# Kernel optimization log

Hardware: AMD Instinct MI355X
Metric: run time of the kernel (lower is better)

The kernel has to match this reference:

```python
import jax, jax.numpy as jnp
import numpy as np

B, TC, TP = 2, 1024, 512
NVC, NVP = 8, 4
D, K, H, DFF, L, HOR, NQ = 128, 3, 8, 512, 2, 96, 3
DK = D // H
MASK_VAL = -1e4  # finite stand-in for -inf; entmax15 support never reaches entries this far below the row max


def entmax15(z):
    # Exact 1.5-entmax over the last axis (Peters & Martins sort-based algorithm).
    z = z / 2.0
    z = z - jnp.max(z, axis=-1, keepdims=True)
    zs = jnp.flip(jnp.sort(z, axis=-1), axis=-1)  # descending
    kk = jnp.arange(1, z.shape[-1] + 1, dtype=z.dtype)
    mean = jnp.cumsum(zs, axis=-1) / kk
    meansq = jnp.cumsum(zs * zs, axis=-1) / kk
    ss = kk * (meansq - mean * mean)
    delta = (1.0 - ss) / kk
    pos = delta > 0
    sqrt_d = jnp.where(pos, jnp.sqrt(jnp.where(pos, delta, 1.0)), 0.0)  # grad-safe sqrt
    tau = mean - sqrt_d
    support = jnp.sum((tau <= zs).astype(jnp.int32), axis=-1, keepdims=True)
    tau_star = jnp.take_along_axis(tau, support - 1, axis=-1)
    return jnp.square(jnp.clip(z - tau_star, 0.0, None))


def layer_norm(x, g, b, eps=1e-5):
    m = jnp.mean(x, axis=-1, keepdims=True)
    v = jnp.mean(jnp.square(x - m), axis=-1, keepdims=True)
    return (x - m) * jax.lax.rsqrt(v + eps) * g + b


def selector(x, conv_w, conv_b, sel_w, sel_b, key):
    # x: [B, T, nv]; causal depthwise-grouped conv -> per-var local states [B, T, nv, D]
    Bs, T, nv = x.shape
    xc = jnp.transpose(x, (0, 2, 1))  # [B, nv, T]
    out = jax.lax.conv_general_dilated(
        xc, conv_w, window_strides=(1,), padding=[(K - 1, 0)],
        dimension_numbers=('NCH', 'OIH', 'NCH'), feature_group_count=nv)
    ls = out.reshape(Bs, nv, D, T) + conv_b[None, :, :, None]
    ls = jnp.transpose(ls, (0, 3, 1, 2))  # [B, T, nv, D]
    scores = ls @ sel_w + sel_b  # [B, T, nv]
    scores = jnp.clip(scores, -10.0, 10.0)
    scores = scores + 1e-4 * jax.random.normal(key, scores.shape, scores.dtype)
    w = entmax15(scores)  # [B, T, nv]
    weighted = jnp.sum(ls * w[..., None], axis=2)  # [B, T, D]
    return weighted, w


def attn_block(x, Wq, bq, Wk, bk, Wv, bv, Wo, bo):
    Bs, T, _ = x.shape
    q = (x @ Wq + bq).reshape(Bs, T, H, DK)
    k = (x @ Wk + bk).reshape(Bs, T, H, DK)
    v = (x @ Wv + bv).reshape(Bs, T, H, DK)
    scores = jnp.einsum('bthd,bshd->bhts', q, k) / jnp.sqrt(jnp.float32(DK))
    mask = jnp.triu(jnp.ones((T, T), bool), 1)
    scores = jnp.where(mask[None, None], MASK_VAL, scores)
    w = entmax15(scores)            # [B, H, T, T]
    w_avg = jnp.mean(w, axis=1)     # [B, T, T]
    v_comb = jnp.mean(v, axis=2)    # [B, T, DK]
    out = jnp.einsum('bts,bsd->btd', w_avg, v_comb)
    return out @ Wo + bo, w_avg


def forward(x_cond, x_pred, cw_c, cb_c, sw_c, sb_c, cw_p, cb_p, sw_p, sb_p,
            Wq, bq, Wk, bk, Wv, bv, Wo, bo, ln1_g, ln1_b,
            fw1, fb1, fw2, fb2, ln2_g, ln2_b, proj_w, proj_b):
    nk = jax.random.key(42)
    xc, v_cond = selector(x_cond, cw_c, cb_c, sw_c, sb_c, jax.random.fold_in(nk, 0))
    xp, v_pred = selector(x_pred, cw_p, cb_p, sw_p, sb_p, jax.random.fold_in(nk, 1))
    x = jnp.concatenate([xc, xp], axis=1)  # [B, TC+TP, D]
    logs = []
    for l in range(L):
        a, w = attn_block(x, Wq[l], bq[l], Wk[l], bk[l], Wv[l], bv[l], Wo[l], bo[l])
        x = layer_norm(x + a, ln1_g[l], ln1_b[l])
        h = jax.nn.relu(x @ fw1[l] + fb1[l])
        x = layer_norm(h @ fw2[l] + fb2[l] + x, ln2_g[l], ln2_b[l])
        logs.append(w)
    seq_last = x[:, -1, :]
    out = jnp.einsum('bd,qdh->bqh', seq_last, proj_w) + proj_b  # [B, NQ, HOR]
    return out, v_cond, v_pred, jnp.stack(logs)


def setup_inputs():
    key = jax.random.key(0)
    ks = jax.random.split(key, 16)
    def w(i, shp):
        return (0.02 * jax.random.normal(ks[i], shp)).astype(jnp.float32)
    z = lambda shp: jnp.zeros(shp, jnp.float32)
    o = lambda shp: jnp.ones(shp, jnp.float32)
    return {
        'x_cond': jax.random.normal(ks[0], (B, TC, NVC), jnp.float32),
        'x_pred': jax.random.normal(ks[1], (B, TP, NVP), jnp.float32),
        'cw_c': w(2, (NVC * D, 1, K)), 'cb_c': z((NVC, D)),
        'sw_c': w(3, (D,)), 'sb_c': z((1,)),
        'cw_p': w(4, (NVP * D, 1, K)), 'cb_p': z((NVP, D)),
        'sw_p': w(5, (D,)), 'sb_p': z((1,)),
        'Wq': w(6, (L, D, D)), 'bq': z((L, D)),
        'Wk': w(7, (L, D, D)), 'bk': z((L, D)),
        'Wv': w(8, (L, D, D)), 'bv': z((L, D)),
        'Wo': w(9, (L, DK, D)), 'bo': z((L, D)),
        'ln1_g': o((L, D)), 'ln1_b': z((L, D)),
        'fw1': w(10, (L, D, DFF)), 'fb1': z((L, DFF)),
        'fw2': w(11, (L, DFF, D)), 'fb2': z((L, D)),
        'ln2_g': o((L, D)), 'ln2_b': z((L, D)),
        'proj_w': w(12, (NQ, D, HOR)), 'proj_b': z((NQ, HOR)),
    }


def reference(x_cond, x_pred, cw_c, cb_c, sw_c, sb_c, cw_p, cb_p, sw_p, sb_p,
              Wq, bq, Wk, bk, Wv, bv, Wo, bo, ln1_g, ln1_b,
              fw1, fb1, fw2, fb2, ln2_g, ln2_b, proj_w, proj_b):
    return forward(x_cond, x_pred, cw_c, cb_c, sw_c, sb_c, cw_p, cb_p, sw_p, sb_p,
                   Wq, bq, Wk, bk, Wv, bv, Wo, bo, ln1_g, ln1_b,
                   fw1, fb1, fw2, fb2, ln2_g, ln2_b, proj_w, proj_b)
```

## Files before the change

kernel.cpp:

```cpp
#include <hip/hip_runtime.h>

namespace {

constexpr int NB_  = 2;
constexpr int TC_  = 1024;
constexpr int TP_  = 512;
constexpr int TT_  = 1536;
constexpr int D_   = 128;
constexpr int H_   = 8;
constexpr int DK_  = 16;
constexpr int DFF_ = 512;
constexpr int L_   = 2;
constexpr int HOR_ = 96;
constexpr int NQ_  = 3;

constexpr int SCP_ = TT_ + 8;

typedef _Float16 h2 __attribute__((ext_vector_type(2)));

constexpr int OFF_OUT  = 0;
constexpr int OFF_VC   = NB_ * NQ_ * HOR_;
constexpr int OFF_VP   = OFF_VC + NB_ * TC_ * 8;
constexpr int OFF_LOGS = OFF_VP + NB_ * TP_ * 4;

constexpr int WS_XA  = 0;
constexpr int WS_XB  = WS_XA  + NB_ * TT_ * D_;
constexpr int WS_Q16 = WS_XB  + NB_ * TT_ * D_;
constexpr int WS_K16 = WS_Q16 + NB_ * TT_ * D_ / 2;
constexpr int WS_VC  = WS_K16 + NB_ * TT_ * D_ / 2;
constexpr int WS_WVC = WS_VC  + NB_ * TT_ * DK_;
constexpr int WS_BVC = WS_WVC + L_ * D_ * DK_;

__device__ inline float dot2f(h2 a, h2 b, float c) {
#if __has_builtin(__builtin_amdgcn_fdot2)
    return __builtin_amdgcn_fdot2(a, b, c, false);
#else
    return c + (float)a[0] * (float)b[0] + (float)a[1] * (float)b[1];
#endif
}

__device__ inline unsigned pack2h(float a, float b) {
#if __has_builtin(__builtin_amdgcn_cvt_pkrtz)
    return __builtin_bit_cast(unsigned, __builtin_amdgcn_cvt_pkrtz(a, b));
#else
    h2 p; p[0] = (_Float16)a; p[1] = (_Float16)b;
    return __builtin_bit_cast(unsigned, p);
#endif
}

__device__ inline float fast_rcp(float x) {
#if __has_builtin(__builtin_amdgcn_rcpf)
    return __builtin_amdgcn_rcpf(x);
#else
    return 1.0f / x;
#endif
}

template <int CTRL>
__device__ inline float dpp_add(float x) {
    const int y = __builtin_amdgcn_update_dpp(
        0, __builtin_bit_cast(int, x), CTRL, 0xF, 0xF, true);
    return x + __builtin_bit_cast(float, y);
}
template <int CTRL>
__device__ inline float dpp_maxf(float x) {
    const int y = __builtin_amdgcn_update_dpp(
        __builtin_bit_cast(int, x), __builtin_bit_cast(int, x),
        CTRL, 0xF, 0xF, false);
    return fmaxf(x, __builtin_bit_cast(float, y));
}
__device__ inline float bcast63(float x) {
    return __builtin_bit_cast(float,
        __builtin_amdgcn_readlane(__builtin_bit_cast(int, x), 63));
}
__device__ inline float wave_sum_l63(float x) {
    x = dpp_add<0x111>(x); x = dpp_add<0x112>(x); x = dpp_add<0x114>(x);
    x = dpp_add<0x118>(x); x = dpp_add<0x142>(x); x = dpp_add<0x143>(x);
    return x;
}
__device__ inline float wave_sum(float x) { return bcast63(wave_sum_l63(x)); }
__device__ inline float wave_max(float x) {
    x = dpp_maxf<0x111>(x); x = dpp_maxf<0x112>(x); x = dpp_maxf<0x114>(x);
    x = dpp_maxf<0x118>(x); x = dpp_maxf<0x142>(x); x = dpp_maxf<0x143>(x);
    return bcast63(x);
}

__global__ __launch_bounds__(128) void prep_wvc_kernel(
    const float* __restrict__ Wv, const float* __restrict__ bv,
    float* __restrict__ wvc, float* __restrict__ bvc)
{
    const int l = blockIdx.x;
    const float* W  = Wv + (long)l * D_ * D_;
    const float* bb = bv + l * D_;
    float* wv = wvc + l * D_ * DK_;
    float* bo = bvc + l * DK_;
    const int tid = threadIdx.x;
    for (int idx = tid; idx < D_ * DK_; idx += 128) {
        const int i = idx >> 4, dk = idx & 15;
        float s = 0.f;
        #pragma unroll
        for (int hh = 0; hh < H_; ++hh) s += W[i * D_ + hh * DK_ + dk];
        wv[idx] = s * 0.125f;
    }
    if (tid < DK_) {
        float s = 0.f;
        #pragma unroll
        for (int hh = 0; hh < H_; ++hh) s += bb[hh * DK_ + tid];
        bo[tid] = s * 0.125f;
    }
}

template <int NV>
__device__ inline void selector_qkv_body(
    const float* __restrict__ x, const float* __restrict__ cw,
    const float* __restrict__ cb, const float* __restrict__ sw,
    const float* __restrict__ sb, float* __restrict__ vout,
    float* __restrict__ xout, int Tsel, int row_off, int blk,
    const float* __restrict__ Wq, const float* __restrict__ bq,
    const float* __restrict__ Wk, const float* __restrict__ bk,
    const float* __restrict__ wvc, const float* __restrict__ bvc,
    _Float16* __restrict__ q16, _Float16* __restrict__ k16,
    float* __restrict__ vc)
{
    const int tpb = Tsel / 4;
    const int b   = blk / tpb;
    const int t0  = (blk - b * tpb) * 4;
    const int tid = threadIdx.x;
    const int lane = tid & 63, wave = tid >> 6;
    const int t = t0 + wave;

    __shared__ float xrT[D_][4];

    const int d0 = lane, d1 = lane + 64;
    float xw[3 * NV];
    #pragma unroll
    for (int kk = 0; kk < 3; ++kk) {
        const int ts = t + kk - 2;
        #pragma unroll
        for (int v = 0; v < NV; ++v)
            xw[kk * NV + v] = (ts >= 0) ? x[((long)b * Tsel + ts) * NV + v] : 0.0f;
    }
    float ls0[NV], ls1[NV];
    #pragma unroll
    for (int v = 0; v < NV; ++v) {
        const float* c0 = cw + ((long)(v * D_ + d0)) * 3;
        const float* c1 = cw + ((long)(v * D_ + d1)) * 3;
        float a0 = cb[v * D_ + d0], a1 = cb[v * D_ + d1];
        a0 = fmaf(xw[0*NV+v], c0[0], a0); a1 = fmaf(xw[0*NV+v], c1[0], a1);
        a0 = fmaf(xw[1*NV+v], c0[1], a0); a1 = fmaf(xw[1*NV+v], c1[1], a1);
        a0 = fmaf(xw[2*NV+v], c0[2], a0); a1 = fmaf(xw[2*NV+v], c1[2], a1);
        ls0[v] = a0; ls1[v] = a1;
    }
    float u[NV];
    {
        const float s0 = sw[d0], s1 = sw[d1];
        #pragma unroll
        for (int v = 0; v < NV; ++v)
            u[v] = wave_sum(fmaf(ls1[v], s1, ls0[v] * s0));
    }
    float wls[NV];
    {
        float m = -1e30f;
        #pragma unroll
        for (int v = 0; v < NV; ++v) {
            float s = u[v] + sb[0];
            s = fminf(fmaxf(s, -10.0f), 10.0f);
            u[v] = 0.5f * s;
            m = fmaxf(m, u[v]);
        }
        float tau = m - 1.0f;
        for (int it = 0; it < 12; ++it) {
            float S1 = 0.f, S2 = 0.f;
            #pragma unroll
            for (int v = 0; v < NV; ++v) {
                float dd = fmaxf(u[v] - tau, 0.f);
                S1 += dd; S2 = fmaf(dd, dd, S2);
            }
            tau += (S2 - 1.0f) * 0.5f * fast_rcp(S1);
        }
        float S1 = 0.f, S2 = 0.f, K = 0.f;
        #pragma unroll
        for (int v = 0; v < NV; ++v) {
            if (u[v] > tau) { S1 += u[v]; S2 = fmaf(u[v], u[v], S2); K += 1.f; }
        }
        const float mean = S1 / K;
        const float arg  = fmaxf(fmaf(mean, mean, -(S2 - 1.0f) / K), 0.f);
        tau = mean - sqrtf(arg);
        #pragma unroll
        for (int v = 0; v < NV; ++v) {
            const float dd = fmaxf(u[v] - tau, 0.f);
            wls[v] = dd * dd;
        }
    }
    float acc0 = 0.f, acc1 = 0.f;
    #pragma unroll
    for (int v = 0; v < NV; ++v) {
        acc0 = fmaf(ls0[v], wls[v], acc0);
        acc1 = fmaf(ls1[v], wls[v], acc1);
    }
    const long rowb = (long)b * TT_ + row_off + t0;
    const long row  = rowb + wave;
    xout[row * D_ + d0] = acc0;
    xout[row * D_ + d1] = acc1;
    xrT[d0][wave] = acc0;
    xrT[d1][wave] = acc1;
    if (lane == 0) {
        #pragma unroll
        for (int v = 0; v < NV; ++v)
            vout[((long)b * Tsel + t) * NV + v] = wls[v];
    }
    __syncthreads();

    {
        const int c = tid & 127;
        const int which = tid >> 7;
        const float* __restrict__ W = which ? Wk : Wq;
        const float bb = which ? bk[c] : bq[c];
        float a0 = bb, a1 = bb, a2 = bb, a3 = bb;
        for (int i = 0; i < D_; ++i) {
            const float wv = W[i * D_ + c];
            const float4 xv = *(const float4*)&xrT[i][0];
            a0 = fmaf(xv.x, wv, a0);
            a1 = fmaf(xv.y, wv, a1);
            a2 = fmaf(xv.z, wv, a2);
            a3 = fmaf(xv.w, wv, a3);
        }
        _Float16* __restrict__ dst = which ? k16 : q16;
        dst[(rowb + 0) * D_ + c] = (_Float16)a0;
        dst[(rowb + 1) * D_ + c] = (_Float16)a1;
        dst[(rowb + 2) * D_ + c] = (_Float16)a2;
        dst[(rowb + 3) * D_ + c] = (_Float16)a3;
    }
    if (tid < 64) {
        const int r = tid >> 4, c16 = tid & 15;
        float av = bvc[c16];
        for (int i = 0; i < D_; ++i)
            av = fmaf(xrT[i][r], wvc[i * DK_ + c16], av);
        vc[(rowb + r) * DK_ + c16] = av;
    }
}

__global__ __launch_bounds__(256) void pre_kernel(
    const float* __restrict__ x_cond, const float* __restrict__ cw_c,
    const float* __restrict__ cb_c, const float* __restrict__ sw_c,
    const float* __restrict__ sb_c,
    const float* __restrict__ x_pred, const float* __restrict__ cw_p,
    const float* __restrict__ cb_p, const float* __restrict__ sw_p,
    const float* __restrict__ sb_p,
    float* __restrict__ vc_out, float* __restrict__ vp_out,
    float* __restrict__ xout,
    const float* __restrict__ Wq, const float* __restrict__ bq,
    const float* __restrict__ Wk, const float* __restrict__ bk,
    const float* __restrict__ wvc, const float* __restrict__ bvc,
    _Float16* __restrict__ q16, _Float16* __restrict__ k16,
    float* __restrict__ vc)
{
    const int blk = blockIdx.x;
    if (blk < NB_ * TC_ / 4) {
        selector_qkv_body<8>(x_cond, cw_c, cb_c, sw_c, sb_c, vc_out, xout,
                             TC_, 0, blk, Wq, bq, Wk, bk, wvc, bvc,
                             q16, k16, vc);
    } else {
        selector_qkv_body<4>(x_pred, cw_p, cb_p, sw_p, sb_p, vp_out, xout,
                             TP_, TC_, blk - NB_ * TC_ / 4,
                             Wq, bq, Wk, bk, wvc, bvc, q16, k16, vc);
    }
}

template <int NJ>
__device__ inline void entmax_head2(unsigned short* __restrict__ sa,
                                    unsigned short* __restrict__ sb,
                                    int lane, int t)
{
    const unsigned* __restrict__ rpa = (const unsigned*)sa;
    const unsigned* __restrict__ rpb = (const unsigned*)sb;
    float va[2 * NJ], vb[2 * NJ];
    #pragma unroll
    for (int j = 0; j < NJ; ++j) {
        const unsigned dwa = rpa[64 * j + lane];
        const unsigned dwb = rpb[64 * j + lane];
        const h2 ha = __builtin_bit_cast(h2, dwa);
        const h2 hb = __builtin_bit_cast(h2, dwb);
        const int s0 = 128 * j + 2 * lane;
        const bool in0 = (s0 <= t), in1 = (s0 + 1 <= t);
        va[2*j]   = in0 ? (float)ha[0] : -1e30f;
        va[2*j+1] = in1 ? (float)ha[1] : -1e30f;
        vb[2*j]   = in0 ? (float)hb[0] : -1e30f;
        vb[2*j+1] = in1 ? (float)hb[1] : -1e30f;
    }

    float ma0 = va[0], ma1 = va[1], mb0 = vb[0], mb1 = vb[1];
    #pragma unroll
    for (int j = 2; j < 2 * NJ; j += 2) {
        ma0 = fmaxf(ma0, va[j]); ma1 = fmaxf(ma1, va[j+1]);
        mb0 = fmaxf(mb0, vb[j]); mb1 = fmaxf(mb1, vb[j+1]);
    }
    const float ma = wave_max(fmaxf(ma0, ma1));
    const float mb = wave_max(fmaxf(mb0, mb1));

    float ta = ma - 1.0f, tb = mb - 1.0f;
    #pragma unroll
    for (int it = 0; it < 7; ++it) {
        float a10 = 0.f, a11 = 0.f, a20 = 0.f, a21 = 0.f;
        float b10 = 0.f, b11 = 0.f, b20 = 0.f, b21 = 0.f;
        #pragma unroll
        for (int j = 0; j < 2 * NJ; j += 2) {
            const float da0 = fmaxf(va[j]   - ta, 0.f);
            const float da1 = fmaxf(va[j+1] - ta, 0.f);
            const float db0 = fmaxf(vb[j]   - tb, 0.f);
            const float db1 = fmaxf(vb[j+1] - tb, 0.f);
            a10 += da0; a11 += da1;
            a20 = fmaf(da0, da0, a20); a21 = fmaf(da1, da1, a21);
            b10 += db0; b11 += db1;
            b20 = fmaf(db0, db0, b20); b21 = fmaf(db1, db1, b21);
        }
        const float S1a = wave_sum(a10 + a11);
        const float S2a = wave_sum(a20 + a21);
        const float S1b = wave_sum(b10 + b11);
        const float S2b = wave_sum(b20 + b21);
        ta += (S2a - 1.0f) * 0.5f * fast_rcp(S1a);
        tb += (S2b - 1.0f) * 0.5f * fast_rcp(S1b);
    }
    {
        float a1 = 0.f, a2 = 0.f, ka = 0.f;
        float b1 = 0.f, b2 = 0.f, kb = 0.f;
        #pragma unroll
        for (int j = 0; j < 2 * NJ; ++j) {
            if (va[j] > ta) { a1 += va[j]; a2 = fmaf(va[j], va[j], a2); ka += 1.f; }
            if (vb[j] > tb) { b1 += vb[j]; b2 = fmaf(vb[j], vb[j], b2); kb += 1.f; }
        }
        a1 = wave_sum(a1); a2 = wave_sum(a2); ka = wave_sum(ka);
        b1 = wave_sum(b1); b2 = wave_sum(b2); kb = wave_sum(kb);
        const float meana = a1 / ka;
        const float arga  = fmaxf(fmaf(meana, meana, -(a2 - 1.0f) / ka), 0.f);
        ta = meana - sqrtf(arga);
        const float meanb = b1 / kb;
        const float argb  = fmaxf(fmaf(meanb, meanb, -(b2 - 1.0f) / kb), 0.f);
        tb = meanb - sqrtf(argb);
    }
    unsigned* __restrict__ wpa = (unsigned*)sa;
    unsigned* __restrict__ wpb = (unsigned*)sb;
    #pragma unroll
    for (int j = 0; j < NJ; ++j) {
        const float da0 = fmaxf(va[2*j]   - ta, 0.f);
        const float da1 = fmaxf(va[2*j+1] - ta, 0.f);
        const float db0 = fmaxf(vb[2*j]   - tb, 0.f);
        const float db1 = fmaxf(vb[2*j+1] - tb, 0.f);
        wpa[64 * j + lane] = pack2h(da0 * da0, da1 * da1);
        wpb[64 * j + lane] = pack2h(db0 * db0, db1 * db1);
    }
}

template <int NJ>
__device__ inline void entmax_pair(unsigned short* __restrict__ scb,
                                   int wave, int lane, int t)
{
    entmax_head2<NJ>(scb + (wave * 2 + 0) * SCP_,
                     scb + (wave * 2 + 1) * SCP_, lane, t);
}

__global__ __launch_bounds__(256) void attn_kernel(
    const _Float16* __restrict__ q16, const _Float16* __restrict__ k16,
    const float* __restrict__ vcomb, const float* __restrict__ xin,
    float* __restrict__ xout,
    const float* __restrict__ Wo, const float* __restrict__ bo,
    const float* __restrict__ lng, const float* __restrict__ lnb,
    float* __restrict__ logs)
{
    __shared__ unsigned short scb[H_ * SCP_];
    __shared__ _Float16 qrow16[D_];
    __shared__ float red[64];
    __shared__ float o16[DK_];
    __shared__ float yrow[D_];
    __shared__ float stat[2];

    const int blk = blockIdx.x;
    const int t = TT_ - 1 - (blk >> 1);
    const int b = blk & 1;
    const int tid = threadIdx.x;
    const int lane = tid & 63, wave = tid >> 6;
    const long rowq  = (long)b * TT_ + t;
    const long bbase = (long)b * TT_;

    if (tid < 64)
        ((unsigned*)qrow16)[tid] = ((const unsigned*)(q16 + rowq * D_))[tid];
    __syncthreads();

    {
        const int h  = tid & 7;
        const int sl = tid >> 3;
        unsigned short* __restrict__ srow = scb + h * SCP_;
        h2 qv[8];
        __builtin_memcpy(qv, (const _Float16*)qrow16 + h * DK_, 32);
        for (int s = sl; s <= t; s += 32) {
            float4 kk0, kk1;
            {
                const float4* kp4 = (const float4*)(k16 + (bbase + s) * D_ + h * DK_);
                kk0 = kp4[0]; kk1 = kp4[1];
            }
            h2 kh[8];
            __builtin_memcpy(kh,     &kk0, 16);
            __builtin_memcpy(kh + 4, &kk1, 16);
            float dot = 0.f;
            #pragma unroll
            for (int i2 = 0; i2 < 8; ++i2) dot = dot2f(qv[i2], kh[i2], dot);
            const _Float16 sh = (_Float16)(dot * 0.125f);
            srow[s] = __builtin_bit_cast(unsigned short, sh);
        }
    }
    __syncthreads();

    {
        const int njn = (t >> 7) + 1;
        switch ((njn + 1) & ~1) {
        case 2:  entmax_pair<2 >(scb, wave, lane, t); break;
        case 4:  entmax_pair<4 >(scb, wave, lane, t); break;
        case 6:  entmax_pair<6 >(scb, wave, lane, t); break;
        case 8:  entmax_pair<8 >(scb, wave, lane, t); break;
        case 10: entmax_pair<10>(scb, wave, lane, t); break;
        default: entmax_pair<12>(scb, wave, lane, t); break;
        }
    }
    __syncthreads();

    float4 A0 = make_float4(0,0,0,0), A1 = A0, A2 = A0, A3 = A0;
    float* lrow = logs + rowq * TT_;
    const unsigned* __restrict__ rp0 = (const unsigned*)scb;
    #pragma unroll
    for (int it = 0; it < 3; ++it) {
        const int dwi = tid + 256 * it;
        const int s0 = 2 * dwi;
        if (s0 <= t) {
            h2 hs = __builtin_bit_cast(h2, rp0[dwi]);
            #pragma unroll
            for (int h = 1; h < H_; ++h)
                hs = hs + __builtin_bit_cast(h2, rp0[h * (SCP_ / 2) + dwi]);
            const float wa0 = (float)hs[0] * 0.125f;
            const float wa1 = (float)hs[1] * 0.125f;
            {
                const float4* vp = (const float4*)(vcomb + (bbase + s0) * DK_);
                const float4 v0 = vp[0], v1 = vp[1], v2 = vp[2], v3 = vp[3];
                A0.x = fmaf(wa0, v0.x, A0.x); A0.y = fmaf(wa0, v0.y, A0.y);
                A0.z = fmaf(wa0, v0.z, A0.z); A0.w = fmaf(wa0, v0.w, A0.w);
                A1.x = fmaf(wa0, v1.x, A1.x); A1.y = fmaf(wa0, v1.y, A1.y);
                A1.z = fmaf(wa0, v1.z, A1.z); A1.w = fmaf(wa0, v1.w, A1.w);
                A2.x = fmaf(wa0, v2.x, A2.x); A2.y = fmaf(wa0, v2.y, A2.y);
                A2.z = fmaf(wa0, v2.z, A2.z); A2.w = fmaf(wa0, v2.w, A2.w);
                A3.x = fmaf(wa0, v3.x, A3.x); A3.y = fmaf(wa0, v3.y, A3.y);
                A3.z = fmaf(wa0, v3.z, A3.z); A3.w = fmaf(wa0, v3.w, A3.w);
            }
            if (s0 + 1 <= t) {
                const float4* vp = (const float4*)(vcomb + (bbase + s0 + 1) * DK_);
                const float4 v0 = vp[0], v1 = vp[1], v2 = vp[2], v3 = vp[3];
                A0.x = fmaf(wa1, v0.x, A0.x); A0.y = fmaf(wa1, v0.y, A0.y);
                A0.z = fmaf(wa1, v0.z, A0.z); A0.w = fmaf(wa1, v0.w, A0.w);
                A1.x = fmaf(wa1, v1.x, A1.x); A1.y = fmaf(wa1, v1.y, A1.y);
                A1.z = fmaf(wa1, v1.z, A1.z); A1.w = fmaf(wa1, v1.w, A1.w);
                A2.x = fmaf(wa1, v2.x, A2.x); A2.y = fmaf(wa1, v2.y, A2.y);
                A2.z = fmaf(wa1, v2.z, A2.z); A2.w = fmaf(wa1, v2.w, A2.w);
                A3.x = fmaf(wa1, v3.x, A3.x); A3.y = fmaf(wa1, v3.y, A3.y);
                A3.z = fmaf(wa1, v3.z, A3.z); A3.w = fmaf(wa1, v3.w, A3.w);
            }
            *(float2*)(lrow + s0) = make_float2(wa0, wa1);
        } else {
            *(float2*)(lrow + s0) = make_float2(0.f, 0.f);
        }
    }
    A0.x = wave_sum_l63(A0.x); A0.y = wave_sum_l63(A0.y);
    A0.z = wave_sum_l63(A0.z); A0.w = wave_sum_l63(A0.w);
    A1.x = wave_sum_l63(A1.x); A1.y = wave_sum_l63(A1.y);
    A1.z = wave_sum_l63(A1.z); A1.w = wave_sum_l63(A1.w);
    A2.x = wave_sum_l63(A2.x); A2.y = wave_sum_l63(A2.y);
    A2.z = wave_sum_l63(A2.z); A2.w = wave_sum_l63(A2.w);
    A3.x = wave_sum_l63(A3.x); A3.y = wave_sum_l63(A3.y);
    A3.w = wave_sum_l63(A3.w); A3.z = wave_sum_l63(A3.z);
    if (lane == 63) {
        float* r = red + wave * 16;
        r[0]=A0.x; r[1]=A0.y; r[2]=A0.z; r[3]=A0.w;
        r[4]=A1.x; r[5]=A1.y; r[6]=A1.z; r[7]=A1.w;
        r[8]=A2.x; r[9]=A2.y; r[10]=A2.z; r[11]=A2.w;
        r[12]=A3.x; r[13]=A3.y; r[14]=A3.z; r[15]=A3.w;
    }
    __syncthreads();
    if (tid < DK_) o16[tid] = red[tid] + red[16 + tid] + red[32 + tid] + red[48 + tid];
    __syncthreads();

    float y = 0.f;
    if (tid < D_) {
        float a = bo[tid];
        #pragma unroll
        for (int j = 0; j < DK_; ++j) a = fmaf(o16[j], Wo[j * D_ + tid], a);
        y = xin[rowq * D_ + tid] + a;
        yrow[tid] = y;
    }
    __syncthreads();
    if (tid < 64) {
        const float y0 = yrow[tid], y1 = yrow[tid + 64];
        float sm = wave_sum_l63(y0 + y1);
        float sq = wave_sum_l63(fmaf(y0, y0, y1 * y1));
        if (tid == 63) {
            const float mean = sm * (1.0f / D_);
            stat[0] = mean;
            stat[1] = fmaxf(sq * (1.0f / D_) - mean * mean, 0.f);
        }
    }
    __syncthreads();
    if (tid < D_) {
        const float r = rsqrtf(stat[1] + 1e-5f);
        xout[rowq * D_ + tid] = (y - stat[0]) * r * lng[tid] + lnb[tid];
    }
}

__global__ __launch_bounds__(256) void ffn_kernel(
    const float* __restrict__ xin, float* __restrict__ xout,
    const float* __restrict__ fw1, const float* __restrict__ fb1,
    const float* __restrict__ fw2, const float* __restrict__ fb2,
    const float* __restrict__ g, const float* __restrict__ bta,
    int do_qkv,
    const float* __restrict__ Wq, const float* __restrict__ bq,
    const float* __restrict__ Wk, const float* __restrict__ bk,
    const float* __restrict__ wvc, const float* __restrict__ bvc,
    _Float16* __restrict__ q16, _Float16* __restrict__ k16,
    float* __restrict__ vc,
    int do_proj, const float* __restrict__ pw,
    const float* __restrict__ pb, float* __restrict__ outp)
{
    __shared__ float xrT[D_][4];
    __shared__ float hbT[DFF_][4];
    __shared__ float pred[2][4][D_];
    __shared__ float yb[4][D_];
    __shared__ float xn[D_];

    const long row0 = (long)blockIdx.x * 4;
    const int tid = threadIdx.x;

    for (int idx = tid; idx < 4 * D_; idx += 256) {
        const int r = idx >> 7, i = idx & 127;
        xrT[i][r] = xin[row0 * D_ + idx];
    }
    __syncthreads();

    {
        const int c = tid;
        float4 a0 = make_float4(0,0,0,0), a1 = a0;
        for (int i = 0; i < D_; ++i) {
            const float w0 = fw1[i * DFF_ + c];
            const float w1 = fw1[i * DFF_ + c + 256];
            const float4 xv = *(const float4*)&xrT[i][0];
            a0.x = fmaf(xv.x, w0, a0.x); a0.y = fmaf(xv.y, w0, a0.y);
            a0.z = fmaf(xv.z, w0, a0.z); a0.w = fmaf(xv.w, w0, a0.w);
            a1.x = fmaf(xv.x, w1, a1.x); a1.y = fmaf(xv.y, w1, a1.y);
            a1.z = fmaf(xv.z, w1, a1.z); a1.w = fmaf(xv.w, w1, a1.w);
        }
        const float b0 = fb1[c], b1 = fb1[c + 256];
        float4 h0, h1;
        h0.x = fmaxf(a0.x + b0, 0.f); h0.y = fmaxf(a0.y + b0, 0.f);
        h0.z = fmaxf(a0.z + b0, 0.f); h0.w = fmaxf(a0.w + b0, 0.f);
        h1.x = fmaxf(a1.x + b1, 0.f); h1.y = fmaxf(a1.y + b1, 0.f);
        h1.z = fmaxf(a1.z + b1, 0.f); h1.w = fmaxf(a1.w + b1, 0.f);
        *(float4*)&hbT[c][0]       = h0;
        *(float4*)&hbT[c + 256][0] = h1;
    }
    __syncthreads();

    {
        const int d = tid & 127;
        const int half = tid >> 7;
        const int j0 = half * 256;
        float a0 = 0.f, a1 = 0.f, a2 = 0.f, a3 = 0.f;
        for (int j = j0; j < j0 + 256; ++j) {
            const float wv = fw2[j * D_ + d];
            const float4 hv = *(const float4*)&hbT[j][0];
            a0 = fmaf(hv.x, wv, a0);
            a1 = fmaf(hv.y, wv, a1);
            a2 = fmaf(hv.z, wv, a2);
            a3 = fmaf(hv.w, wv, a3);
        }
        pred[half][0][d] = a0; pred[half][1][d] = a1;
        pred[half][2][d] = a2; pred[half][3][d] = a3;
    }
    __syncthreads();

    {
        const int d = tid & 127;
        const int r0 = (tid >> 7) * 2;
        const float bb = fb2[d];
        yb[r0 + 0][d] = pred[0][r0 + 0][d] + pred[1][r0 + 0][d] + bb + xrT[d][r0 + 0];
        yb[r0 + 1][d] = pred[0][r0 + 1][d] + pred[1][r0 + 1][d] + bb + xrT[d][r0 + 1];
    }
    __syncthreads();

    const int w = tid >> 6, lane = tid & 63;
    const bool pblk = do_proj && (((row0 + 4) % TT_) == 0);
    {
        const float y0 = yb[w][lane], y1 = yb[w][lane + 64];
        const float sm = wave_sum(y0 + y1);
        const float sq = wave_sum(fmaf(y0, y0, y1 * y1));
        const float mean = sm * (1.0f / D_);
        const float var  = fmaxf(sq * (1.0f / D_) - mean * mean, 0.f);
        const float rcp = rsqrtf(var + 1e-5f);
        const float o0 = (y0 - mean) * rcp * g[lane]      + bta[lane];
        const float o1 = (y1 - mean) * rcp * g[lane + 64] + bta[lane + 64];
        xout[(row0 + w) * D_ + lane]      = o0;
        xout[(row0 + w) * D_ + lane + 64] = o1;
        xrT[lane][w]      = o0;
        xrT[lane + 64][w] = o1;
        if (pblk && w == 3) { xn[lane] = o0; xn[lane + 64] = o1; }
    }

    if (do_qkv) {
        __syncthreads();
        const int c = tid & 127;
        const int which = tid >> 7;
        const float* __restrict__ W = which ? Wk : Wq;
        const float bb = which ? bk[c] : bq[c];
        float a0 = bb, a1 = bb, a2 = bb, a3 = bb;
        for (int i = 0; i < D_; ++i) {
            const float wv = W[i * D_ + c];
            const float4 xv = *(const float4*)&xrT[i][0];
            a0 = fmaf(xv.x, wv, a0);
            a1 = fmaf(xv.y, wv, a1);
            a2 = fmaf(xv.z, wv, a2);
            a3 = fmaf(xv.w, wv, a3);
        }
        _Float16* __restrict__ dst = which ? k16 : q16;
        dst[(row0 + 0) * D_ + c] = (_Float16)a0;
        dst[(row0 + 1) * D_ + c] = (_Float16)a1;
        dst[(row0 + 2) * D_ + c] = (_Float16)a2;
        dst[(row0 + 3) * D_ + c] = (_Float16)a3;

        if (tid < 64) {
            const int r = tid >> 4, c16 = tid & 15;
            float av = bvc[c16];
            for (int i = 0; i < D_; ++i)
                av = fmaf(xrT[i][r], wvc[i * DK_ + c16], av);
            vc[(row0 + r) * DK_ + c16] = av;
        }
    }

    if (pblk) {
        __syncthreads();
        const int b = (int)((row0 + 3) / TT_);
        for (int idx = tid; idx < NQ_ * HOR_; idx += 256) {
            const int qq = idx / HOR_, hh = idx - qq * HOR_;
            float s = pb[idx];
            for (int d = 0; d < D_; ++d)
                s = fmaf(xn[d], pw[((long)qq * D_ + d) * HOR_ + hh], s);
            outp[b * NQ_ * HOR_ + idx] = s;
        }
    }
}

}

extern "C" void kernel_launch(void* const* d_in, const int* in_sizes, int n_in,
                              void* d_out, int out_size, void* d_ws, size_t ws_size,
                              hipStream_t stream) {
    (void)in_sizes; (void)n_in; (void)out_size; (void)ws_size;

    const float* x_cond = (const float*)d_in[0];
    const float* x_pred = (const float*)d_in[1];
    const float* cw_c   = (const float*)d_in[2];
    const float* cb_c   = (const float*)d_in[3];
    const float* sw_c   = (const float*)d_in[4];
    const float* sb_c   = (const float*)d_in[5];
    const float* cw_p   = (const float*)d_in[6];
    const float* cb_p   = (const float*)d_in[7];
    const float* sw_p   = (const float*)d_in[8];
    const float* sb_p   = (const float*)d_in[9];
    const float* Wq     = (const float*)d_in[10];
    const float* bq     = (const float*)d_in[11];
    const float* Wk     = (const float*)d_in[12];
    const float* bk     = (const float*)d_in[13];
    const float* Wv     = (const float*)d_in[14];
    const float* bv     = (const float*)d_in[15];
    const float* Wo     = (const float*)d_in[16];
    const float* bo     = (const float*)d_in[17];
    const float* ln1g   = (const float*)d_in[18];
    const float* ln1b   = (const float*)d_in[19];
    const float* fw1    = (const float*)d_in[20];
    const float* fb1    = (const float*)d_in[21];
    const float* fw2    = (const float*)d_in[22];
    const float* fb2    = (const float*)d_in[23];
    const float* ln2g   = (const float*)d_in[24];
    const float* ln2b   = (const float*)d_in[25];
    const float* pw     = (const float*)d_in[26];
    const float* pb     = (const float*)d_in[27];

    float* outp = (float*)d_out;
    float* ws   = (float*)d_ws;
    float*     xA   = ws + WS_XA;
    float*     xB   = ws + WS_XB;
    _Float16*  q16  = (_Float16*)(ws + WS_Q16);
    _Float16*  k16  = (_Float16*)(ws + WS_K16);
    float*     vcb  = ws + WS_VC;
    float*     wvc  = ws + WS_WVC;
    float*     bvc  = ws + WS_BVC;

    prep_wvc_kernel<<<L_, 128, 0, stream>>>(Wv, bv, wvc, bvc);

    pre_kernel<<<(NB_ * TC_ + NB_ * TP_) / 4, 256, 0, stream>>>(
        x_cond, cw_c, cb_c, sw_c, sb_c,
        x_pred, cw_p, cb_p, sw_p, sb_p,
        outp + OFF_VC, outp + OFF_VP, xA,
        Wq, bq, Wk, bk, wvc, bvc, q16, k16, vcb);

    for (int l = 0; l < L_; ++l) {
        attn_kernel<<<NB_ * TT_, 256, 0, stream>>>(
            q16, k16, vcb, xA, xB,
            Wo + (long)l * DK_ * D_, bo + l * D_,
            ln1g + l * D_, ln1b + l * D_,
            outp + OFF_LOGS + (long)l * NB_ * TT_ * TT_);
        const int nl = l + 1;
        ffn_kernel<<<NB_ * TT_ / 4, 256, 0, stream>>>(
            xB, xA, fw1 + (long)l * D_ * DFF_, fb1 + l * DFF_,
            fw2 + (long)l * DFF_ * D_, fb2 + l * D_,
            ln2g + l * D_, ln2b + l * D_,
            (l < L_ - 1) ? 1 : 0,
            Wq + (long)nl * D_ * D_ * (l < L_ - 1),
            bq + nl * D_ * (l < L_ - 1),
            Wk + (long)nl * D_ * D_ * (l < L_ - 1),
            bk + nl * D_ * (l < L_ - 1),
            wvc + nl * D_ * DK_ * (l < L_ - 1),
            bvc + nl * DK_ * (l < L_ - 1),
            q16, k16, vcb,
            (l == L_ - 1) ? 1 : 0, pw, pb, outp);
    }
}
```

Measured before the change: 300.2 us.

## Pack FFN and Q/K weights to fp16 pairs and use dot2 accumulation

A widened prep kernel converts fw1, fw2, Wq and Wk into packed half2 layouts, pairing adjacent reduction rows. The FFN and QKV projection loops then run on fp16 dot2 instructions over packed activations in shared memory. This halves weight bytes and instruction count in those loops. In exchange it adds an fp16 rounding step and a per-call conversion pass, plus extra syncs to pack activations.

```diff
diff --git a/kernel.cpp b/kernel.cpp
--- a/kernel.cpp
+++ b/kernel.cpp
@@ -30,6 +30,13 @@
 constexpr int WS_VC  = WS_K16 + NB_ * TT_ * D_ / 2;
 constexpr int WS_WVC = WS_VC  + NB_ * TT_ * DK_;
 constexpr int WS_BVC = WS_WVC + L_ * D_ * DK_;
+constexpr int FH1_L  = (D_ / 2) * DFF_;
+constexpr int FH2_L  = (DFF_ / 2) * D_;
+constexpr int WHQ_L  = (D_ / 2) * D_;
+constexpr int WS_FH1 = WS_BVC + L_ * DK_;
+constexpr int WS_FH2 = WS_FH1 + L_ * FH1_L;
+constexpr int WS_WHQ = WS_FH2 + L_ * FH2_L;
+constexpr int WS_WHK = WS_WHQ + L_ * WHQ_L;
 
 __device__ inline float dot2f(h2 a, h2 b, float c) {
 #if __has_builtin(__builtin_amdgcn_fdot2)
@@ -85,28 +92,53 @@
     return bcast63(x);
 }
 
-__global__ __launch_bounds__(128) void prep_wvc_kernel(
+__global__ __launch_bounds__(256) void prep_kernel(
     const float* __restrict__ Wv, const float* __restrict__ bv,
-    float* __restrict__ wvc, float* __restrict__ bvc)
+    float* __restrict__ wvc, float* __restrict__ bvc,
+    const float* __restrict__ fw1, const float* __restrict__ fw2,
+    const float* __restrict__ Wq, const float* __restrict__ Wk,
+    unsigned* __restrict__ fh1, unsigned* __restrict__ fh2,
+    unsigned* __restrict__ whq, unsigned* __restrict__ whk)
 {
-    const int l = blockIdx.x;
-    const float* W  = Wv + (long)l * D_ * D_;
-    const float* bb = bv + l * D_;
-    float* wv = wvc + l * D_ * DK_;
-    float* bo = bvc + l * DK_;
-    const int tid = threadIdx.x;
-    for (int idx = tid; idx < D_ * DK_; idx += 128) {
-        const int i = idx >> 4, dk = idx & 15;
+    const int gid = blockIdx.x * 256 + threadIdx.x;
+    const int stride = gridDim.x * 256;
+
+    for (int e = gid; e < L_ * D_ * DK_; e += stride) {
+        const int l = e / (D_ * DK_), rem = e - l * D_ * DK_;
+        const int i = rem >> 4, dk = rem & 15;
+        const float* W = Wv + (long)l * D_ * D_;
         float s = 0.f;
         #pragma unroll
         for (int hh = 0; hh < H_; ++hh) s += W[i * D_ + hh * DK_ + dk];
-        wv[idx] = s * 0.125f;
-    }
-    if (tid < DK_) {
+        wvc[e] = s * 0.125f;
+    }
+    for (int e = gid; e < L_ * DK_; e += stride) {
+        const int l = e / DK_, dk = e - l * DK_;
+        const float* bb = bv + l * D_;
         float s = 0.f;
         #pragma unroll
-        for (int hh = 0; hh < H_; ++hh) s += bb[hh * DK_ + tid];
-        bo[tid] = s * 0.125f;
+        for (int hh = 0; hh < H_; ++hh) s += bb[hh * DK_ + dk];
+        bvc[e] = s * 0.125f;
+    }
+    for (int e = gid; e < L_ * FH1_L; e += stride) {
+        const int l = e / FH1_L, rem = e - l * FH1_L;
+        const int i2 = rem / DFF_, c = rem - i2 * DFF_;
+        const float* W = fw1 + (long)l * D_ * DFF_;
+        fh1[e] = pack2h(W[(2 * i2) * DFF_ + c], W[(2 * i2 + 1) * DFF_ + c]);
+    }
+    for (int e = gid; e < L_ * FH2_L; e += stride) {
+        const int l = e / FH2_L, rem = e - l * FH2_L;
+        const int j2 = rem >> 7, d = rem & 127;
+        const float* W = fw2 + (long)l * DFF_ * D_;
+        fh2[e] = pack2h(W[(2 * j2) * D_ + d], W[(2 * j2 + 1) * D_ + d]);
+    }
+    for (int e = gid; e < L_ * WHQ_L; e += stride) {
+        const int l = e / WHQ_L, rem = e - l * WHQ_L;
+        const int i2 = rem >> 7, c = rem & 127;
+        const float* Q = Wq + (long)l * D_ * D_;
+        const float* K = Wk + (long)l * D_ * D_;
+        whq[e] = pack2h(Q[(2 * i2) * D_ + c], Q[(2 * i2 + 1) * D_ + c]);
+        whk[e] = pack2h(K[(2 * i2) * D_ + c], K[(2 * i2 + 1) * D_ + c]);
     }
 }
 
@@ -116,8 +148,8 @@
     const float* __restrict__ cb, const float* __restrict__ sw,
     const float* __restrict__ sb, float* __restrict__ vout,
     float* __restrict__ xout, int Tsel, int row_off, int blk,
-    const float* __restrict__ Wq, const float* __restrict__ bq,
-    const float* __restrict__ Wk, const float* __restrict__ bk,
+    const unsigned* __restrict__ whq0, const float* __restrict__ bq,
+    const unsigned* __restrict__ whk0, const float* __restrict__ bk,
     const float* __restrict__ wvc, const float* __restrict__ bvc,
     _Float16* __restrict__ q16, _Float16* __restrict__ k16,
     float* __restrict__ vc)
@@ -130,6 +162,7 @@
     const int t = t0 + wave;
 
     __shared__ float xrT[D_][4];
+    __shared__ unsigned xh2[D_ / 2][4];
 
     const int d0 = lane, d1 = lane + 64;
     float xw[3 * NV];
@@ -212,18 +245,24 @@
     __syncthreads();
 
     {
+        const int i2 = tid >> 2, r = tid & 3;
+        xh2[i2][r] = pack2h(xrT[2 * i2][r], xrT[2 * i2 + 1][r]);
+    }
+    __syncthreads();
+
+    {
         const int c = tid & 127;
         const int which = tid >> 7;
-        const float* __restrict__ W = which ? Wk : Wq;
+        const unsigned* __restrict__ Wp = which ? whk0 : whq0;
         const float bb = which ? bk[c] : bq[c];
         float a0 = bb, a1 = bb, a2 = bb, a3 = bb;
-        for (int i = 0; i < D_; ++i) {
-            const float wv = W[i * D_ + c];
-            const float4 xv = *(const float4*)&xrT[i][0];
-            a0 = fmaf(xv.x, wv, a0);
-            a1 = fmaf(xv.y, wv, a1);
-            a2 = fmaf(xv.z, wv, a2);
-            a3 = fmaf(xv.w, wv, a3);
+        for (int i2 = 0; i2 < D_ / 2; ++i2) {
+            const h2 w = __builtin_bit_cast(h2, Wp[i2 * D_ + c]);
+            const uint4 xp = *(const uint4*)&xh2[i2][0];
+            a0 = dot2f(w, __builtin_bit_cast(h2, xp.x), a0);
+            a1 = dot2f(w, __builtin_bit_cast(h2, xp.y), a1);
+            a2 = dot2f(w, __builtin_bit_cast(h2, xp.z), a2);
+            a3 = dot2f(w, __builtin_bit_cast(h2, xp.w), a3);
         }
         _Float16* __restrict__ dst = which ? k16 : q16;
         dst[(rowb + 0) * D_ + c] = (_Float16)a0;
@@ -249,8 +288,8 @@
     const float* __restrict__ sb_p,
     float* __restrict__ vc_out, float* __restrict__ vp_out,
     float* __restrict__ xout,
-    const float* __restrict__ Wq, const float* __restrict__ bq,
-    const float* __restrict__ Wk, const float* __restrict__ bk,
+    const unsigned* __restrict__ whq0, const float* __restrict__ bq,
+    const unsigned* __restrict__ whk0, const float* __restrict__ bk,
     const float* __restrict__ wvc, const float* __restrict__ bvc,
     _Float16* __restrict__ q16, _Float16* __restrict__ k16,
     float* __restrict__ vc)
@@ -258,12 +297,12 @@
     const int blk = blockIdx.x;
     if (blk < NB_ * TC_ / 4) {
         selector_qkv_body<8>(x_cond, cw_c, cb_c, sw_c, sb_c, vc_out, xout,
-                             TC_, 0, blk, Wq, bq, Wk, bk, wvc, bvc,
+                             TC_, 0, blk, whq0, bq, whk0, bk, wvc, bvc,
                              q16, k16, vc);
     } else {
         selector_qkv_body<4>(x_pred, cw_p, cb_p, sw_p, sb_p, vp_out, xout,
                              TP_, TC_, blk - NB_ * TC_ / 4,
-                             Wq, bq, Wk, bk, wvc, bvc, q16, k16, vc);
+                             whq0, bq, whk0, bk, wvc, bvc, q16, k16, vc);
     }
 }
 
@@ -473,7 +512,7 @@
     A2.x = wave_sum_l63(A2.x); A2.y = wave_sum_l63(A2.y);
     A2.z = wave_sum_l63(A2.z); A2.w = wave_sum_l63(A2.w);
     A3.x = wave_sum_l63(A3.x); A3.y = wave_sum_l63(A3.y);
-    A3.w = wave_sum_l63(A3.w); A3.z = wave_sum_l63(A3.z);
+    A3.z = wave_sum_l63(A3.z); A3.w = wave_sum_l63(A3.w);
     if (lane == 63) {
         float* r = red + wave * 16;
         r[0]=A0.x; r[1]=A0.y; r[2]=A0.z; r[3]=A0.w;
@@ -513,12 +552,12 @@
 
 __global__ __launch_bounds__(256) void ffn_kernel(
     const float* __restrict__ xin, float* __restrict__ xout,
-    const float* __restrict__ fw1, const float* __restrict__ fb1,
-    const float* __restrict__ fw2, const float* __restrict__ fb2,
+    const unsigned* __restrict__ fh1l, const float* __restrict__ fb1,
+    const unsigned* __restrict__ fh2l, const float* __restrict__ fb2,
     const float* __restrict__ g, const float* __restrict__ bta,
     int do_qkv,
-    const float* __restrict__ Wq, const float* __restrict__ bq,
-    const float* __restrict__ Wk, const float* __restrict__ bk,
+    const unsigned* __restrict__ whq_nl, const float* __restrict__ bq,
+    const unsigned* __restrict__ whk_nl, const float* __restrict__ bk,
     const float* __restrict__ wvc, const float* __restrict__ bvc,
     _Float16* __restrict__ q16, _Float16* __restrict__ k16,
     float* __restrict__ vc,
@@ -526,7 +565,8 @@
     const float* __restrict__ pb, float* __restrict__ outp)
 {
     __shared__ float xrT[D_][4];
-    __shared__ float hbT[DFF_][4];
+    __shared__ unsigned xh2[D_ / 2][4];
+    __shared__ unsigned hb2[4 * (DFF_ / 2)];
     __shared__ float pred[2][4][D_];
     __shared__ float yb[4][D_];
     __shared__ float xn[D_];
@@ -539,42 +579,48 @@
         xrT[i][r] = xin[row0 * D_ + idx];
     }
     __syncthreads();
-
-    {
-        const int c = tid;
-        float4 a0 = make_float4(0,0,0,0), a1 = a0;
-        for (int i = 0; i < D_; ++i) {
-            const float w0 = fw1[i * DFF_ + c];
-            const float w1 = fw1[i * DFF_ + c + 256];
-            const float4 xv = *(const float4*)&xrT[i][0];
-            a0.x = fmaf(xv.x, w0, a0.x); a0.y = fmaf(xv.y, w0, a0.y);
-            a0.z = fmaf(xv.z, w0, a0.z); a0.w = fmaf(xv.w, w0, a0.w);
-            a1.x = fmaf(xv.x, w1, a1.x); a1.y = fmaf(xv.y, w1, a1.y);
-            a1.z = fmaf(xv.z, w1, a1.z); a1.w = fmaf(xv.w, w1, a1.w);
-        }
-        const float b0 = fb1[c], b1 = fb1[c + 256];
-        float4 h0, h1;
-        h0.x = fmaxf(a0.x + b0, 0.f); h0.y = fmaxf(a0.y + b0, 0.f);
-        h0.z = fmaxf(a0.z + b0, 0.f); h0.w = fmaxf(a0.w + b0, 0.f);
-        h1.x = fmaxf(a1.x + b1, 0.f); h1.y = fmaxf(a1.y + b1, 0.f);
-        h1.z = fmaxf(a1.z + b1, 0.f); h1.w = fmaxf(a1.w + b1, 0.f);
-        *(float4*)&hbT[c][0]       = h0;
-        *(float4*)&hbT[c + 256][0] = h1;
+    {
+        const int i2 = tid >> 2, r = tid & 3;
+        xh2[i2][r] = pack2h(xrT[2 * i2][r], xrT[2 * i2 + 1][r]);
+    }
+    __syncthreads();
+
+    {
+        const int c2 = tid;
+        const uint2* __restrict__ wp2 = (const uint2*)fh1l;
+        float4 aE = make_float4(0,0,0,0), aO = aE;
+        for (int i2 = 0; i2 < D_ / 2; ++i2) {
+            const uint2 w = wp2[i2 * 256 + c2];
+            const h2 wE = __builtin_bit_cast(h2, w.x);
+            const h2 wO = __builtin_bit_cast(h2, w.y);
+            const uint4 xp = *(const uint4*)&xh2[i2][0];
+            const h2 x0 = __builtin_bit_cast(h2, xp.x);
+            const h2 x1 = __builtin_bit_cast(h2, xp.y);
+            const h2 x2 = __builtin_bit_cast(h2, xp.z);
+            const h2 x3 = __builtin_bit_cast(h2, xp.w);
+            aE.x = dot2f(wE, x0, aE.x); aE.y = dot2f(wE, x1, aE.y);
+            aE.z = dot2f(wE, x2, aE.z); aE.w = dot2f(wE, x3, aE.w);
+            aO.x = dot2f(wO, x0, aO.x); aO.y = dot2f(wO, x1, aO.y);
+            aO.z = dot2f(wO, x2, aO.z); aO.w = dot2f(wO, x3, aO.w);
+        }
+        const float bE = fb1[2 * c2], bO = fb1[2 * c2 + 1];
+        hb2[0 * 256 + c2] = pack2h(fmaxf(aE.x + bE, 0.f), fmaxf(aO.x + bO, 0.f));
+        hb2[1 * 256 + c2] = pack2h(fmaxf(aE.y + bE, 0.f), fmaxf(aO.y + bO, 0.f));
+        hb2[2 * 256 + c2] = pack2h(fmaxf(aE.z + bE, 0.f), fmaxf(aO.z + bO, 0.f));
+        hb2[3 * 256 + c2] = pack2h(fmaxf(aE.w + bE, 0.f), fmaxf(aO.w + bO, 0.f));
     }
     __syncthreads();
 
     {
         const int d = tid & 127;
         const int half = tid >> 7;
-        const int j0 = half * 256;
         float a0 = 0.f, a1 = 0.f, a2 = 0.f, a3 = 0.f;
-        for (int j = j0; j < j0 + 256; ++j) {
-            const float wv = fw2[j * D_ + d];
-            const float4 hv = *(const float4*)&hbT[j][0];
-            a0 = fmaf(hv.x, wv, a0);
-            a1 = fmaf(hv.y, wv, a1);
-            a2 = fmaf(hv.z, wv, a2);
-            a3 = fmaf(hv.w, wv, a3);
+        for (int j2 = half * 128; j2 < half * 128 + 128; ++j2) {
+            const h2 w = __builtin_bit_cast(h2, fh2l[j2 * D_ + d]);
+            a0 = dot2f(w, __builtin_bit_cast(h2, hb2[0 * 256 + j2]), a0);
+            a1 = dot2f(w, __builtin_bit_cast(h2, hb2[1 * 256 + j2]), a1);
+            a2 = dot2f(w, __builtin_bit_cast(h2, hb2[2 * 256 + j2]), a2);
+            a3 = dot2f(w, __builtin_bit_cast(h2, hb2[3 * 256 + j2]), a3);
         }
         pred[half][0][d] = a0; pred[half][1][d] = a1;
         pred[half][2][d] = a2; pred[half][3][d] = a3;
@@ -610,18 +656,23 @@
 
     if (do_qkv) {
         __syncthreads();
+        {
+            const int i2 = tid >> 2, r = tid & 3;
+            xh2[i2][r] = pack2h(xrT[2 * i2][r], xrT[2 * i2 + 1][r]);
+        }
+        __syncthreads();
         const int c = tid & 127;
         const int which = tid >> 7;
-        const float* __restrict__ W = which ? Wk : Wq;
+        const unsigned* __restrict__ Wp = which ? whk_nl : whq_nl;
         const float bb = which ? bk[c] : bq[c];
         float a0 = bb, a1 = bb, a2 = bb, a3 = bb;
-        for (int i = 0; i < D_; ++i) {
-            const float wv = W[i * D_ + c];
-            const float4 xv = *(const float4*)&xrT[i][0];
-            a0 = fmaf(xv.x, wv, a0);
-            a1 = fmaf(xv.y, wv, a1);
-            a2 = fmaf(xv.z, wv, a2);
-            a3 = fmaf(xv.w, wv, a3);
+        for (int i2 = 0; i2 < D_ / 2; ++i2) {
+            const h2 wv = __builtin_bit_cast(h2, Wp[i2 * D_ + c]);
+            const uint4 xp = *(const uint4*)&xh2[i2][0];
+            a0 = dot2f(wv, __builtin_bit_cast(h2, xp.x), a0);
+            a1 = dot2f(wv, __builtin_bit_cast(h2, xp.y), a1);
+            a2 = dot2f(wv, __builtin_bit_cast(h2, xp.z), a2);
+            a3 = dot2f(wv, __builtin_bit_cast(h2, xp.w), a3);
         }
         _Float16* __restrict__ dst = which ? k16 : q16;
         dst[(row0 + 0) * D_ + c] = (_Float16)a0;
@@ -696,14 +747,20 @@
     float*     vcb  = ws + WS_VC;
     float*     wvc  = ws + WS_WVC;
     float*     bvc  = ws + WS_BVC;
-
-    prep_wvc_kernel<<<L_, 128, 0, stream>>>(Wv, bv, wvc, bvc);
+    unsigned*  fh1  = (unsigned*)(ws + WS_FH1);
+    unsigned*  fh2  = (unsigned*)(ws + WS_FH2);
+    unsigned*  whq  = (unsigned*)(ws + WS_WHQ);
+    unsigned*  whk  = (unsigned*)(ws + WS_WHK);
+
+    prep_kernel<<<128, 256, 0, stream>>>(Wv, bv, wvc, bvc,
+                                         fw1, fw2, Wq, Wk,
+                                         fh1, fh2, whq, whk);
 
     pre_kernel<<<(NB_ * TC_ + NB_ * TP_) / 4, 256, 0, stream>>>(
         x_cond, cw_c, cb_c, sw_c, sb_c,
         x_pred, cw_p, cb_p, sw_p, sb_p,
         outp + OFF_VC, outp + OFF_VP, xA,
-        Wq, bq, Wk, bk, wvc, bvc, q16, k16, vcb);
+        whq, bq, whk, bk, wvc, bvc, q16, k16, vcb);
 
     for (int l = 0; l < L_; ++l) {
         attn_kernel<<<NB_ * TT_, 256, 0, stream>>>(
@@ -712,17 +769,15 @@
             ln1g + l * D_, ln1b + l * D_,
             outp + OFF_LOGS + (long)l * NB_ * TT_ * TT_);
         const int nl = l + 1;
+        const int more = (l < L_ - 1);
         ffn_kernel<<<NB_ * TT_ / 4, 256, 0, stream>>>(
-            xB, xA, fw1 + (long)l * D_ * DFF_, fb1 + l * DFF_,
-            fw2 + (long)l * DFF_ * D_, fb2 + l * D_,
+            xB, xA, fh1 + (long)l * FH1_L, fb1 + l * DFF_,
+            fh2 + (long)l * FH2_L, fb2 + l * D_,
             ln2g + l * D_, ln2b + l * D_,
-            (l < L_ - 1) ? 1 : 0,
-            Wq + (long)nl * D_ * D_ * (l < L_ - 1),
-            bq + nl * D_ * (l < L_ - 1),
-            Wk + (long)nl * D_ * D_ * (l < L_ - 1),
-            bk + nl * D_ * (l < L_ - 1),
-            wvc + nl * D_ * DK_ * (l < L_ - 1),
-            bvc + nl * DK_ * (l < L_ - 1),
+            more,
+            whq + (long)nl * WHQ_L * more, bq + nl * D_ * more,
+            whk + (long)nl * WHQ_L * more, bk + nl * D_ * more,
+            wvc + nl * D_ * DK_ * more, bvc + nl * DK_ * more,
             q16, k16, vcb,
             (l == L_ - 1) ? 1 : 0, pw, pb, outp);
     }
```

Result: slower. 335.6 us (+11.8%).
